# Kernel optimization log

Hardware: AMD Instinct MI355X
Metric: run time of the kernel (lower is better)

## Reference

```python
import jax, jax.numpy as jnp
import numpy as np

N_NODES = 100000
N_EDGES = 1600000
IN_FEATS = 128
N_HIDDEN = 128
N_CLASSES = 16


def setup_inputs() -> dict:
    key = jax.random.key(0)
    ks = jax.random.split(key, 10)
    features = jax.random.normal(ks[0], (N_NODES, IN_FEATS), dtype=jnp.float32)
    src = jax.random.randint(ks[1], (N_EDGES,), 0, N_NODES, dtype=jnp.int32)
    dst = jax.random.randint(ks[2], (N_EDGES,), 0, N_NODES, dtype=jnp.int32)
    # Glorot-ish init for the three GraphConv layers
    def glorot(k, fan_in, fan_out):
        s = (2.0 / (fan_in + fan_out)) ** 0.5
        return jax.random.normal(k, (fan_in, fan_out), dtype=jnp.float32) * s
    W0 = glorot(ks[3], IN_FEATS, N_HIDDEN)
    b0 = jnp.zeros((N_HIDDEN,), jnp.float32)
    W1 = glorot(ks[4], N_HIDDEN, N_HIDDEN)
    b1 = jnp.zeros((N_HIDDEN,), jnp.float32)
    W2 = glorot(ks[5], N_HIDDEN, N_CLASSES)
    b2 = jnp.zeros((N_CLASSES,), jnp.float32)
    return {"features": features, "src": src, "dst": dst,
            "W0": W0, "b0": b0, "W1": W1, "b1": b1, "W2": W2, "b2": b2}


def _graph_conv(h, src, dst, src_norm, dst_norm, W, b, act):
    # DGL GraphConv, norm='both':
    # out = D_dst^{-1/2} * sum_{(u->v) in E} (D_src^{-1/2} h)_u W  + b
    h = h * src_norm[:, None]           # [N, F] scale by out-degree^-1/2
    hw = h @ W                          # [N, F_out] transform before gather (F_out <= F here)
    agg = jax.ops.segment_sum(hw[src], dst, num_segments=h.shape[0])  # scatter-add over edges
    out = agg * dst_norm[:, None] + b
    return act(out)


def reference(features, src, dst, W0, b0, W1, b1, W2, b2):
    N = features.shape[0]
    ones = jnp.ones(src.shape[0], dtype=jnp.float32)
    out_deg = jnp.clip(jax.ops.segment_sum(ones, src, num_segments=N), 1.0)
    in_deg = jnp.clip(jax.ops.segment_sum(ones, dst, num_segments=N), 1.0)
    src_norm = out_deg ** -0.5
    dst_norm = in_deg ** -0.5

    relu = jax.nn.relu
    pos_sigmoid = lambda x: jax.nn.sigmoid(x) + 1e-8

    h = features.astype(jnp.float32)
    h = _graph_conv(h, src, dst, src_norm, dst_norm, W0, b0, relu)
    h = _graph_conv(h, src, dst, src_norm, dst_norm, W1, b1, relu)
    h = _graph_conv(h, src, dst, src_norm, dst_norm, W2, b2, pos_sigmoid)
    return h
```

## Files before the change

### kernel.cpp

```cpp
#include <hip/hip_runtime.h>
#include <hip/hip_bf16.h>


constexpr int BLK = 256;
constexpr int CH = 8192;

typedef __attribute__((ext_vector_type(8))) short s8v;
typedef __attribute__((ext_vector_type(4))) float f4v;

__device__ __forceinline__ float bflo(unsigned int u) { return __uint_as_float(u << 16); }
__device__ __forceinline__ float bfhi(unsigned int u) { return __uint_as_float(u & 0xffff0000u); }
__device__ __forceinline__ unsigned int bfr(float f) {
    unsigned int u = __float_as_uint(f);
    return (u + 0x7fffu + ((u >> 16) & 1u)) >> 16;
}
__device__ __forceinline__ unsigned int bfpack(float lo, float hi) {
    unsigned int ul = __float_as_uint(lo), uh = __float_as_uint(hi);
    unsigned int rl = (ul + 0x7fffu + ((ul >> 16) & 1u)) >> 16;
    unsigned int rh = (uh + 0x7fffu + ((uh >> 16) & 1u)) & 0xffff0000u;
    return rl | rh;
}

__global__ __launch_bounds__(256) void k_pcount(const int* __restrict__ src, const int* __restrict__ dst,
                                                int* __restrict__ pmat_d, int* __restrict__ pmat_s,
                                                int E, int NB) {
    __shared__ int hd[1024], hs[1024];
    for (int i = threadIdx.x; i < 1024; i += 256) { hd[i] = 0; hs[i] = 0; }
    __syncthreads();
    int b = blockIdx.x;
    int e0 = b * CH, e1 = min(e0 + CH, E);
    for (int e = e0 + threadIdx.x; e < e1; e += 256) {
        atomicAdd(&hd[dst[e] >> 7], 1);
        atomicAdd(&hs[src[e] >> 7], 1);
    }
    __syncthreads();
    for (int i = threadIdx.x; i < NB; i += 256) {
        pmat_d[(size_t)b * NB + i] = hd[i];
        pmat_s[(size_t)b * NB + i] = hs[i];
    }
}

__global__ __launch_bounds__(1024) void k_pscan1(const int* __restrict__ pmat_d, const int* __restrict__ pmat_s,
                                                 int* __restrict__ bbase_d, int* __restrict__ bbase_s,
                                                 int NB, int nblk) {
    const int* pmat = blockIdx.x ? pmat_s : pmat_d;
    int* bbase = blockIdx.x ? bbase_s : bbase_d;
    __shared__ int s[1024];
    int t = threadIdx.x;
    int tot = 0;
    if (t < NB) {
#pragma unroll 8
        for (int b = 0; b < nblk; b++) tot += pmat[(size_t)b * NB + t];
    }
    s[t] = (t < NB) ? tot : 0;
    __syncthreads();
    for (int d = 1; d < 1024; d <<= 1) {
        int x = (t >= d) ? s[t - d] : 0;
        __syncthreads();
        s[t] += x;
        __syncthreads();
    }
    if (t < NB) {
        bbase[t] = s[t] - tot;
        if (t == NB - 1) bbase[NB] = s[t];
    }
}

__global__ __launch_bounds__(256) void k_pscan2(const int* __restrict__ pmat_d, const int* __restrict__ pmat_s,
                                                const int* __restrict__ bbase_d, const int* __restrict__ bbase_s,
                                                int* __restrict__ omat_d, int* __restrict__ omat_s,
                                                int NB, int nblk) {
    int which = blockIdx.x & 1;
    int t = (blockIdx.x >> 1) * 256 + threadIdx.x;
    const int* pmat = which ? pmat_s : pmat_d;
    const int* bbase = which ? bbase_s : bbase_d;
    int* omat = which ? omat_s : omat_d;
    if (t >= NB) return;
    int run = bbase[t];
#pragma unroll 8
    for (int b = 0; b < nblk; b++) {
        size_t idx = (size_t)b * NB + t;
        omat[idx] = run;
        run += pmat[idx];
    }
}

__global__ __launch_bounds__(256) void k_pscatter(const int* __restrict__ src, const int* __restrict__ dst,
                                                  const int* __restrict__ omat_d, const int* __restrict__ omat_s,
                                                  unsigned int* __restrict__ ebuf_d, unsigned char* __restrict__ ebuf_s,
                                                  int E, int NB) {
    __shared__ int cd[1024], cs[1024];
    int b = blockIdx.x;
    for (int i = threadIdx.x; i < NB; i += 256) {
        cd[i] = omat_d[(size_t)b * NB + i];
        cs[i] = omat_s[(size_t)b * NB + i];
    }
    __syncthreads();
    int e0 = b * CH, e1 = min(e0 + CH, E);
    for (int e = e0 + threadIdx.x; e < e1; e += 256) {
        int s_ = src[e], d_ = dst[e];
        int pd = atomicAdd(&cd[d_ >> 7], 1);
        ebuf_d[pd] = (unsigned)s_ | ((unsigned)(d_ & 127) << 17);
        int ps = atomicAdd(&cs[s_ >> 7], 1);
        ebuf_s[ps] = (unsigned char)(s_ & 127);
    }
}

__global__ __launch_bounds__(256) void k_bcount(const unsigned char* __restrict__ ebuf_s,
                                                const int* __restrict__ bbase_s,
                                                float* __restrict__ srcn, int N) {
    __shared__ int cnt[128];
    int k = blockIdx.x;
    if (threadIdx.x < 128) cnt[threadIdx.x] = 0;
    __syncthreads();
    int beg = bbase_s[k], end = bbase_s[k + 1];
    for (int i = beg + threadIdx.x; i < end; i += 256) atomicAdd(&cnt[ebuf_s[i]], 1);
    __syncthreads();
    if (threadIdx.x < 128) {
        int v = k * 128 + threadIdx.x;
        if (v < N) {
            int c = cnt[threadIdx.x];
            if (c < 1) c = 1;
            srcn[v] = rsqrtf((float)c);
        }
    }
}

__global__ __launch_bounds__(256) void k_sortcsr(const unsigned int* __restrict__ ebuf,
                                                 const int* __restrict__ bbase,
                                                 int* __restrict__ csr, int* __restrict__ rowptr,
                                                 int N, int E) {
    __shared__ unsigned int rec[4096];
    __shared__ unsigned int sorted[4096];
    __shared__ int cnt[128];
    __shared__ int wstart[129];
    __shared__ int wcur[128];
    int k = blockIdx.x, tx = threadIdx.x;
    int ebeg = bbase[k];
    int ecnt = bbase[k + 1] - ebeg;
    if (ecnt > 4096) ecnt = 4096;
    if (tx < 128) cnt[tx] = 0;
    __syncthreads();
    for (int i = tx; i < ecnt; i += 256) {
        unsigned int r = ebuf[ebeg + i];
        rec[i] = r;
        atomicAdd(&cnt[(r >> 17) & 127], 1);
    }
    __syncthreads();
    if (tx < 128) wcur[tx] = cnt[tx];
    __syncthreads();
    for (int d = 1; d < 128; d <<= 1) {
        int x = (tx < 128 && tx >= d) ? wcur[tx - d] : 0;
        __syncthreads();
        if (tx < 128) wcur[tx] += x;
        __syncthreads();
    }
    if (tx < 128) wstart[tx] = wcur[tx] - cnt[tx];
    if (tx == 127) wstart[128] = wcur[127];
    __syncthreads();
    if (tx < 128) wcur[tx] = wstart[tx];
    __syncthreads();
    for (int i = tx; i < ecnt; i += 256) {
        unsigned int r = rec[i];
        int p = atomicAdd(&wcur[(r >> 17) & 127], 1);
        sorted[p] = r & 0x1FFFFu;
    }
    __syncthreads();
    for (int i = tx; i < ecnt; i += 256) csr[ebeg + i] = (int)sorted[i];
    if (tx < 128) {
        int v = k * 128 + tx;
        if (v < N) rowptr[v] = ebeg + wstart[tx];
    }
    if (k == (int)gridDim.x - 1 && tx == 0) rowptr[N] = E;
}

__global__ void k_wt3(const float* __restrict__ W0, const float* __restrict__ W1, const float* __restrict__ W2,
                      unsigned short* __restrict__ Wt0, unsigned short* __restrict__ Wt1,
                      unsigned short* __restrict__ Wt2) {
    int b = blockIdx.x;
    const float* W; unsigned short* Wt; int total, base;
    if (b < 64)      { W = W0; Wt = Wt0; total = 16384; base = b * 256; }
    else if (b < 128){ W = W1; Wt = Wt1; total = 16384; base = (b - 64) * 256; }
    else             { W = W2; Wt = Wt2; total = 2048;  base = (b - 128) * 256; }
    int i = base + threadIdx.x;
    if (i < total) {
        int Ncol = total >> 7;
        int c = i >> 7, k = i & 127;
        Wt[i] = (unsigned short)bfr(W[k * Ncol + c]);
    }
}

template <int NT, int F32IN>
__global__ __launch_bounds__(256) void k_gemm_mfma(const unsigned short* __restrict__ Ab,
                                                   const float* __restrict__ Af,
                                                   const float* __restrict__ srcn,
                                                   const unsigned short* __restrict__ Wt,
                                                   unsigned short* __restrict__ outb, int M) {
    __shared__ unsigned short As[64 * 128];
    __shared__ unsigned short Ws[NT * 16 * 128];
    int tx = threadIdx.x;
    int row0 = blockIdx.x * 64;
    for (int p = 0; p < NT; ++p) {
        int r = p * 16 + (tx >> 4);
        int c = tx & 15;
        int cs = c ^ (r & 7);
        *(uint4*)(&Ws[(r * 16 + cs) * 8]) = *(const uint4*)(Wt + (size_t)r * 128 + c * 8);
    }
    for (int p = 0; p < 4; ++p) {
        int r = p * 16 + (tx >> 4);
        int c = tx & 15;
        int cs = c ^ (r & 7);
        int gr = row0 + r;
        uint4 v = make_uint4(0u, 0u, 0u, 0u);
        if (gr < M) {
            if (F32IN) {
                const float4* pf = (const float4*)(Af + (size_t)gr * 128 + c * 8);
                float4 a = pf[0], b = pf[1];
                float s = srcn[gr];
                v.x = bfpack(a.x * s, a.y * s);
                v.y = bfpack(a.z * s, a.w * s);
                v.z = bfpack(b.x * s, b.y * s);
                v.w = bfpack(b.z * s, b.w * s);
            } else {
                v = *(const uint4*)(Ab + (size_t)gr * 128 + c * 8);
            }
        }
        *(uint4*)(&As[(r * 16 + cs) * 8]) = v;
    }
    __syncthreads();

    int w = tx >> 6, l = tx & 63;
    int lr = l & 15, lg = l >> 4;
    f4v acc[NT];
#pragma unroll
    for (int nt = 0; nt < NT; ++nt) { acc[nt][0] = 0.f; acc[nt][1] = 0.f; acc[nt][2] = 0.f; acc[nt][3] = 0.f; }

    int ar = w * 16 + lr;
#pragma unroll
    for (int kk = 0; kk < 4; ++kk) {
        s8v af = *(const s8v*)(&As[(ar * 16 + ((kk * 4 + lg) ^ (ar & 7))) * 8]);
#pragma unroll
        for (int nt = 0; nt < NT; ++nt) {
            int br = nt * 16 + lr;
            s8v bf = *(const s8v*)(&Ws[(br * 16 + ((kk * 4 + lg) ^ (br & 7))) * 8]);
            acc[nt] = __builtin_amdgcn_mfma_f32_16x16x32_bf16(af, bf, acc[nt], 0, 0, 0);
        }
    }
#pragma unroll
    for (int nt = 0; nt < NT; ++nt) {
#pragma unroll
        for (int i = 0; i < 4; ++i) {
            int R = row0 + w * 16 + lg * 4 + i;
            if (R < M) {
                int col = nt * 16 + lr;
                outb[(size_t)R * (NT * 16) + col] = (unsigned short)bfr(acc[nt][i]);
            }
        }
    }
}

__global__ __launch_bounds__(256) void k_aggN(const unsigned short* __restrict__ hw,
                                              const int* __restrict__ csr,
                                              const int* __restrict__ rowptr,
                                              const float* __restrict__ srcn,
                                              const float* __restrict__ bias,
                                              unsigned short* __restrict__ out, int N) {
    int t = blockIdx.x * 256 + threadIdx.x;
    int v = t >> 4, sub = t & 15;
    if (v >= N) return;
    int s0 = rowptr[v], s1 = rowptr[v + 1];

    float a0 = 0.f, a1 = 0.f, a2 = 0.f, a3 = 0.f, a4 = 0.f, a5 = 0.f, a6 = 0.f, a7 = 0.f;
#define ACC8(V)                                                         \
    a0 += bflo(V.x); a1 += bfhi(V.x); a2 += bflo(V.y); a3 += bfhi(V.y); \
    a4 += bflo(V.z); a5 += bfhi(V.z); a6 += bflo(V.w); a7 += bfhi(V.w);
    int e = s0;
    for (; e + 4 <= s1; e += 4) {
        int x0 = csr[e], x1 = csr[e + 1], x2 = csr[e + 2], x3 = csr[e + 3];
        uint4 v0 = *(const uint4*)(hw + (size_t)x0 * 128 + sub * 8);
        uint4 v1 = *(const uint4*)(hw + (size_t)x1 * 128 + sub * 8);
        uint4 v2 = *(const uint4*)(hw + (size_t)x2 * 128 + sub * 8);
        uint4 v3 = *(const uint4*)(hw + (size_t)x3 * 128 + sub * 8);
        ACC8(v0) ACC8(v1) ACC8(v2) ACC8(v3)
    }
    for (; e < s1; ++e) {
        int x0 = csr[e];
        uint4 v0 = *(const uint4*)(hw + (size_t)x0 * 128 + sub * 8);
        ACC8(v0)
    }
#undef ACC8
    int deg = s1 - s0;
    if (deg < 1) deg = 1;
    float dn = rsqrtf((float)deg);
    float4 b0 = *(const float4*)(bias + sub * 8);
    float4 b1 = *(const float4*)(bias + sub * 8 + 4);
    float sn = srcn[v];
    float o0 = fmaxf(a0 * dn + b0.x, 0.f) * sn, o1 = fmaxf(a1 * dn + b0.y, 0.f) * sn;
    float o2 = fmaxf(a2 * dn + b0.z, 0.f) * sn, o3 = fmaxf(a3 * dn + b0.w, 0.f) * sn;
    float o4 = fmaxf(a4 * dn + b1.x, 0.f) * sn, o5 = fmaxf(a5 * dn + b1.y, 0.f) * sn;
    float o6 = fmaxf(a6 * dn + b1.z, 0.f) * sn, o7 = fmaxf(a7 * dn + b1.w, 0.f) * sn;
    uint4 o;
    o.x = bfpack(o0, o1); o.y = bfpack(o2, o3);
    o.z = bfpack(o4, o5); o.w = bfpack(o6, o7);
    *(uint4*)(out + (size_t)v * 128 + sub * 8) = o;
}

__global__ __launch_bounds__(256) void k_agg16(const unsigned short* __restrict__ hw,
                                               const int* __restrict__ csr,
                                               const int* __restrict__ rowptr,
                                               const float* __restrict__ bias,
                                               float* __restrict__ out, int N) {
    int t = blockIdx.x * 256 + threadIdx.x;
    int v = t >> 2, q = t & 3;
    if (v >= N) return;
    int s0 = rowptr[v], s1 = rowptr[v + 1];
    float a0 = 0.f, a1 = 0.f, a2 = 0.f, a3 = 0.f;
#define ACC4(V)                                                         \
    a0 += bflo(V.x); a1 += bfhi(V.x); a2 += bflo(V.y); a3 += bfhi(V.y);
    int e = s0;
    for (; e + 4 <= s1; e += 4) {
        int x0 = csr[e], x1 = csr[e + 1], x2 = csr[e + 2], x3 = csr[e + 3];
        uint2 v0 = *(const uint2*)(hw + (size_t)x0 * 16 + q * 4);
        uint2 v1 = *(const uint2*)(hw + (size_t)x1 * 16 + q * 4);
        uint2 v2 = *(const uint2*)(hw + (size_t)x2 * 16 + q * 4);
        uint2 v3 = *(const uint2*)(hw + (size_t)x3 * 16 + q * 4);
        ACC4(v0) ACC4(v1) ACC4(v2) ACC4(v3)
    }
    for (; e < s1; ++e) {
        int x0 = csr[e];
        uint2 v0 = *(const uint2*)(hw + (size_t)x0 * 16 + q * 4);
        ACC4(v0)
    }
#undef ACC4
    int deg = s1 - s0;
    if (deg < 1) deg = 1;
    float dn = rsqrtf((float)deg);
    float4 b = *(const float4*)(bias + q * 4);
    float o0 = 1.f / (1.f + __expf(-(a0 * dn + b.x))) + 1e-8f;
    float o1 = 1.f / (1.f + __expf(-(a1 * dn + b.y))) + 1e-8f;
    float o2 = 1.f / (1.f + __expf(-(a2 * dn + b.z))) + 1e-8f;
    float o3 = 1.f / (1.f + __expf(-(a3 * dn + b.w))) + 1e-8f;
    *(float4*)(out + (size_t)v * 16 + q * 4) = make_float4(o0, o1, o2, o3);
}

extern "C" void kernel_launch(void* const* d_in, const int* in_sizes, int n_in,
                              void* d_out, int out_size, void* d_ws, size_t ws_size,
                              hipStream_t stream) {
    const float* features = (const float*)d_in[0];
    const int*   src      = (const int*)d_in[1];
    const int*   dst      = (const int*)d_in[2];
    const float* W0       = (const float*)d_in[3];
    const float* b0       = (const float*)d_in[4];
    const float* W1       = (const float*)d_in[5];
    const float* b1       = (const float*)d_in[6];
    const float* W2       = (const float*)d_in[7];
    const float* b2       = (const float*)d_in[8];
    float* out = (float*)d_out;

    const int N = in_sizes[0] / 128;
    const int E = in_sizes[1];
    const int NB = (N + 127) >> 7;
    const int nblk = (E + CH - 1) / CH;

    char* ws = (char*)d_ws;
    size_t off = 0;
    auto alloc = [&](size_t bytes) -> char* {
        char* p = ws + off;
        off += (bytes + 255) / 256 * 256;
        return p;
    };
    int* pmat_d  = (int*)alloc((size_t)nblk * NB * 4);
    int* pmat_s  = (int*)alloc((size_t)nblk * NB * 4);
    int* omat_d  = (int*)alloc((size_t)nblk * NB * 4);
    int* omat_s  = (int*)alloc((size_t)nblk * NB * 4);
    int* bbase_d = (int*)alloc((size_t)(NB + 1) * 4);
    int* bbase_s = (int*)alloc((size_t)(NB + 1) * 4);
    unsigned int*  ebuf_d = (unsigned int*)alloc((size_t)E * 4);
    unsigned char* ebuf_s = (unsigned char*)alloc((size_t)E);
    int* csr     = (int*)alloc((size_t)E * 4);
    int* rowptr  = (int*)alloc((size_t)(N + 1) * 4);
    float* srcn  = (float*)alloc((size_t)N * 4);
    unsigned short* Wt0 = (unsigned short*)alloc(128 * 128 * 2);
    unsigned short* Wt1 = (unsigned short*)alloc(128 * 128 * 2);
    unsigned short* Wt2 = (unsigned short*)alloc(16 * 128 * 2);
    unsigned short* B1 = (unsigned short*)alloc((size_t)N * 128 * 2);
    unsigned short* B2 = (unsigned short*)alloc((size_t)N * 128 * 2);
    unsigned short* HW16 = (unsigned short*)alloc((size_t)N * 16 * 2);
    (void)ws_size; (void)n_in; (void)out_size;

    k_pcount<<<nblk, 256, 0, stream>>>(src, dst, pmat_d, pmat_s, E, NB);
    k_pscan1<<<2, 1024, 0, stream>>>(pmat_d, pmat_s, bbase_d, bbase_s, NB, nblk);
    k_pscan2<<<2 * ((NB + 255) / 256), 256, 0, stream>>>(pmat_d, pmat_s, bbase_d, bbase_s, omat_d, omat_s, NB, nblk);
    k_pscatter<<<nblk, 256, 0, stream>>>(src, dst, omat_d, omat_s, ebuf_d, ebuf_s, E, NB);
    k_bcount<<<NB, 256, 0, stream>>>(ebuf_s, bbase_s, srcn, N);
    k_sortcsr<<<NB, 256, 0, stream>>>(ebuf_d, bbase_d, csr, rowptr, N, E);
    k_wt3<<<136, 256, 0, stream>>>(W0, W1, W2, Wt0, Wt1, Wt2);

    int gb = (N + 63) / 64;
    int anb = (N * 16 + 255) / 256;
    int a16b = (N * 4 + 255) / 256;

    k_gemm_mfma<8, 1><<<gb, 256, 0, stream>>>(nullptr, features, srcn, Wt0, B2, N);
    k_aggN<<<anb, 256, 0, stream>>>(B2, csr, rowptr, srcn, b0, B1, N);
    k_gemm_mfma<8, 0><<<gb, 256, 0, stream>>>(B1, nullptr, nullptr, Wt1, B2, N);
    k_aggN<<<anb, 256, 0, stream>>>(B2, csr, rowptr, srcn, b1, B1, N);
    k_gemm_mfma<1, 0><<<gb, 256, 0, stream>>>(B1, nullptr, nullptr, Wt2, HW16, N);
    k_agg16<<<a16b, 256, 0, stream>>>(HW16, csr, rowptr, b2, out, N);
}
```

Before: 351.7 us.

## Sort nodes by in-degree for aggregation and load GEMM A operands directly

Adds a counting sort of nodes by in-degree (histogram, scan, scatter) that produces a permutation, so that the aggregation kernels process nodes with similar degree together and wavefront divergence shrinks. The GEMM now reads A fragments straight from global memory into registers instead of staging them in LDS, and each wave computes two 16-row tiles, so a block covers 128 rows. The aggN gather loop is unrolled from 4 to 8 loads to keep more memory requests in flight. This costs three extra small launches, and the permuted order makes node accesses in aggregation less contiguous.

```diff
diff --git a/kernel.cpp b/kernel.cpp
--- a/kernel.cpp
+++ b/kernel.cpp
@@ -4,6 +4,7 @@
 
 constexpr int BLK = 256;
 constexpr int CH = 8192;
+constexpr int DCH = 8192;
 
 typedef __attribute__((ext_vector_type(8))) short s8v;
 typedef __attribute__((ext_vector_type(4))) float f4v;
@@ -174,6 +175,52 @@
     if (k == (int)gridDim.x - 1 && tx == 0) rowptr[N] = E;
 }
 
+__global__ __launch_bounds__(256) void k_dhist(const int* __restrict__ rowptr, int* __restrict__ dpart, int N) {
+    __shared__ int h[128];
+    if (threadIdx.x < 128) h[threadIdx.x] = 0;
+    __syncthreads();
+    int n0 = blockIdx.x * DCH, n1 = min(n0 + DCH, N);
+    for (int n = n0 + threadIdx.x; n < n1; n += 256) {
+        int deg = rowptr[n + 1] - rowptr[n];
+        atomicAdd(&h[min(deg, 127)], 1);
+    }
+    __syncthreads();
+    if (threadIdx.x < 128) dpart[blockIdx.x * 128 + threadIdx.x] = h[threadIdx.x];
+}
+
+__global__ __launch_bounds__(128) void k_dscan(const int* __restrict__ dpart, int* __restrict__ dmat, int nchunk) {
+    __shared__ int s[128];
+    int t = threadIdx.x;
+    int tot = 0;
+    for (int b = 0; b < nchunk; b++) tot += dpart[b * 128 + t];
+    s[t] = tot;
+    __syncthreads();
+    for (int d = 1; d < 128; d <<= 1) {
+        int x = (t >= d) ? s[t - d] : 0;
+        __syncthreads();
+        s[t] += x;
+        __syncthreads();
+    }
+    int run = s[t] - tot;
+    for (int b = 0; b < nchunk; b++) {
+        dmat[b * 128 + t] = run;
+        run += dpart[b * 128 + t];
+    }
+}
+
+__global__ __launch_bounds__(256) void k_dscatter(const int* __restrict__ rowptr, const int* __restrict__ dmat,
+                                                  int* __restrict__ perm, int N) {
+    __shared__ int cur[128];
+    if (threadIdx.x < 128) cur[threadIdx.x] = dmat[blockIdx.x * 128 + threadIdx.x];
+    __syncthreads();
+    int n0 = blockIdx.x * DCH, n1 = min(n0 + DCH, N);
+    for (int n = n0 + threadIdx.x; n < n1; n += 256) {
+        int deg = rowptr[n + 1] - rowptr[n];
+        int p = atomicAdd(&cur[min(deg, 127)], 1);
+        perm[p] = n;
+    }
+}
+
 __global__ void k_wt3(const float* __restrict__ W0, const float* __restrict__ W1, const float* __restrict__ W2,
                       unsigned short* __restrict__ Wt0, unsigned short* __restrict__ Wt1,
                       unsigned short* __restrict__ Wt2) {
@@ -196,64 +243,73 @@
                                                    const float* __restrict__ srcn,
                                                    const unsigned short* __restrict__ Wt,
                                                    unsigned short* __restrict__ outb, int M) {
-    __shared__ unsigned short As[64 * 128];
     __shared__ unsigned short Ws[NT * 16 * 128];
     int tx = threadIdx.x;
-    int row0 = blockIdx.x * 64;
     for (int p = 0; p < NT; ++p) {
         int r = p * 16 + (tx >> 4);
         int c = tx & 15;
         int cs = c ^ (r & 7);
         *(uint4*)(&Ws[(r * 16 + cs) * 8]) = *(const uint4*)(Wt + (size_t)r * 128 + c * 8);
     }
-    for (int p = 0; p < 4; ++p) {
-        int r = p * 16 + (tx >> 4);
-        int c = tx & 15;
-        int cs = c ^ (r & 7);
-        int gr = row0 + r;
-        uint4 v = make_uint4(0u, 0u, 0u, 0u);
-        if (gr < M) {
-            if (F32IN) {
-                const float4* pf = (const float4*)(Af + (size_t)gr * 128 + c * 8);
-                float4 a = pf[0], b = pf[1];
-                float s = srcn[gr];
-                v.x = bfpack(a.x * s, a.y * s);
-                v.y = bfpack(a.z * s, a.w * s);
-                v.z = bfpack(b.x * s, b.y * s);
-                v.w = bfpack(b.z * s, b.w * s);
-            } else {
-                v = *(const uint4*)(Ab + (size_t)gr * 128 + c * 8);
-            }
-        }
-        *(uint4*)(&As[(r * 16 + cs) * 8]) = v;
-    }
     __syncthreads();
 
     int w = tx >> 6, l = tx & 63;
     int lr = l & 15, lg = l >> 4;
-    f4v acc[NT];
-#pragma unroll
-    for (int nt = 0; nt < NT; ++nt) { acc[nt][0] = 0.f; acc[nt][1] = 0.f; acc[nt][2] = 0.f; acc[nt][3] = 0.f; }
-
-    int ar = w * 16 + lr;
+    int row_base = blockIdx.x * 128;
+    int r0 = row_base + (w * 2 + 0) * 16 + lr;
+    int r1 = row_base + (w * 2 + 1) * 16 + lr;
+    bool m0 = r0 < M, m1 = r1 < M;
+    float sn0 = 1.f, sn1 = 1.f;
+    if (F32IN) { sn0 = m0 ? srcn[r0] : 0.f; sn1 = m1 ? srcn[r1] : 0.f; }
+
+    f4v acc[2][NT];
+#pragma unroll
+    for (int s = 0; s < 2; ++s)
+#pragma unroll
+        for (int nt = 0; nt < NT; ++nt) { acc[s][nt][0] = 0.f; acc[s][nt][1] = 0.f; acc[s][nt][2] = 0.f; acc[s][nt][3] = 0.f; }
+
 #pragma unroll
     for (int kk = 0; kk < 4; ++kk) {
-        s8v af = *(const s8v*)(&As[(ar * 16 + ((kk * 4 + lg) ^ (ar & 7))) * 8]);
+        int off = (kk * 4 + lg) * 8;
+        union { uint4 u; s8v v; } a0, a1;
+        a0.u = make_uint4(0u, 0u, 0u, 0u);
+        a1.u = make_uint4(0u, 0u, 0u, 0u);
+        if (F32IN) {
+            if (m0) {
+                const float4* pf = (const float4*)(Af + (size_t)r0 * 128 + off);
+                float4 x = pf[0], y = pf[1];
+                a0.u.x = bfpack(x.x * sn0, x.y * sn0); a0.u.y = bfpack(x.z * sn0, x.w * sn0);
+                a0.u.z = bfpack(y.x * sn0, y.y * sn0); a0.u.w = bfpack(y.z * sn0, y.w * sn0);
+            }
+            if (m1) {
+                const float4* pf = (const float4*)(Af + (size_t)r1 * 128 + off);
+                float4 x = pf[0], y = pf[1];
+                a1.u.x = bfpack(x.x * sn1, x.y * sn1); a1.u.y = bfpack(x.z * sn1, x.w * sn1);
+                a1.u.z = bfpack(y.x * sn1, y.y * sn1); a1.u.w = bfpack(y.z * sn1, y.w * sn1);
+            }
+        } else {
+            if (m0) a0.u = *(const uint4*)(Ab + (size_t)r0 * 128 + off);
+            if (m1) a1.u = *(const uint4*)(Ab + (size_t)r1 * 128 + off);
+        }
 #pragma unroll
         for (int nt = 0; nt < NT; ++nt) {
             int br = nt * 16 + lr;
             s8v bf = *(const s8v*)(&Ws[(br * 16 + ((kk * 4 + lg) ^ (br & 7))) * 8]);
-            acc[nt] = __builtin_amdgcn_mfma_f32_16x16x32_bf16(af, bf, acc[nt], 0, 0, 0);
+            acc[0][nt] = __builtin_amdgcn_mfma_f32_16x16x32_bf16(a0.v, bf, acc[0][nt], 0, 0, 0);
+            acc[1][nt] = __builtin_amdgcn_mfma_f32_16x16x32_bf16(a1.v, bf, acc[1][nt], 0, 0, 0);
         }
     }
 #pragma unroll
-    for (int nt = 0; nt < NT; ++nt) {
-#pragma unroll
-        for (int i = 0; i < 4; ++i) {
-            int R = row0 + w * 16 + lg * 4 + i;
-            if (R < M) {
-                int col = nt * 16 + lr;
-                outb[(size_t)R * (NT * 16) + col] = (unsigned short)bfr(acc[nt][i]);
+    for (int s = 0; s < 2; ++s) {
+#pragma unroll
+        for (int nt = 0; nt < NT; ++nt) {
+#pragma unroll
+            for (int i = 0; i < 4; ++i) {
+                int R = row_base + (w * 2 + s) * 16 + lg * 4 + i;
+                if (R < M) {
+                    int col = nt * 16 + lr;
+                    outb[(size_t)R * (NT * 16) + col] = (unsigned short)bfr(acc[s][nt][i]);
+                }
             }
         }
     }
@@ -262,30 +318,38 @@
 __global__ __launch_bounds__(256) void k_aggN(const unsigned short* __restrict__ hw,
                                               const int* __restrict__ csr,
                                               const int* __restrict__ rowptr,
+                                              const int* __restrict__ perm,
                                               const float* __restrict__ srcn,
                                               const float* __restrict__ bias,
                                               unsigned short* __restrict__ out, int N) {
     int t = blockIdx.x * 256 + threadIdx.x;
-    int v = t >> 4, sub = t & 15;
-    if (v >= N) return;
+    int vi = t >> 4, sub = t & 15;
+    if (vi >= N) return;
+    int v = perm[vi];
     int s0 = rowptr[v], s1 = rowptr[v + 1];
+    const unsigned short* hws = hw + sub * 8;
 
     float a0 = 0.f, a1 = 0.f, a2 = 0.f, a3 = 0.f, a4 = 0.f, a5 = 0.f, a6 = 0.f, a7 = 0.f;
 #define ACC8(V)                                                         \
     a0 += bflo(V.x); a1 += bfhi(V.x); a2 += bflo(V.y); a3 += bfhi(V.y); \
     a4 += bflo(V.z); a5 += bfhi(V.z); a6 += bflo(V.w); a7 += bfhi(V.w);
     int e = s0;
-    for (; e + 4 <= s1; e += 4) {
-        int x0 = csr[e], x1 = csr[e + 1], x2 = csr[e + 2], x3 = csr[e + 3];
-        uint4 v0 = *(const uint4*)(hw + (size_t)x0 * 128 + sub * 8);
-        uint4 v1 = *(const uint4*)(hw + (size_t)x1 * 128 + sub * 8);
-        uint4 v2 = *(const uint4*)(hw + (size_t)x2 * 128 + sub * 8);
-        uint4 v3 = *(const uint4*)(hw + (size_t)x3 * 128 + sub * 8);
-        ACC8(v0) ACC8(v1) ACC8(v2) ACC8(v3)
+    for (; e + 8 <= s1; e += 8) {
+        int x0 = csr[e],     x1 = csr[e + 1], x2 = csr[e + 2], x3 = csr[e + 3];
+        int x4 = csr[e + 4], x5 = csr[e + 5], x6 = csr[e + 6], x7 = csr[e + 7];
+        uint4 v0 = *(const uint4*)(hws + (size_t)x0 * 128);
+        uint4 v1 = *(const uint4*)(hws + (size_t)x1 * 128);
+        uint4 v2 = *(const uint4*)(hws + (size_t)x2 * 128);
+        uint4 v3 = *(const uint4*)(hws + (size_t)x3 * 128);
+        uint4 v4 = *(const uint4*)(hws + (size_t)x4 * 128);
+        uint4 v5 = *(const uint4*)(hws + (size_t)x5 * 128);
+        uint4 v6 = *(const uint4*)(hws + (size_t)x6 * 128);
+        uint4 v7 = *(const uint4*)(hws + (size_t)x7 * 128);
+        ACC8(v0) ACC8(v1) ACC8(v2) ACC8(v3) ACC8(v4) ACC8(v5) ACC8(v6) ACC8(v7)
     }
     for (; e < s1; ++e) {
         int x0 = csr[e];
-        uint4 v0 = *(const uint4*)(hw + (size_t)x0 * 128 + sub * 8);
+        uint4 v0 = *(const uint4*)(hws + (size_t)x0 * 128);
         ACC8(v0)
     }
 #undef ACC8
@@ -308,27 +372,30 @@
 __global__ __launch_bounds__(256) void k_agg16(const unsigned short* __restrict__ hw,
                                                const int* __restrict__ csr,
                                                const int* __restrict__ rowptr,
+                                               const int* __restrict__ perm,
                                                const float* __restrict__ bias,
                                                float* __restrict__ out, int N) {
     int t = blockIdx.x * 256 + threadIdx.x;
-    int v = t >> 2, q = t & 3;
-    if (v >= N) return;
+    int vi = t >> 2, q = t & 3;
+    if (vi >= N) return;
+    int v = perm[vi];
     int s0 = rowptr[v], s1 = rowptr[v + 1];
+    const unsigned short* hws = hw + q * 4;
     float a0 = 0.f, a1 = 0.f, a2 = 0.f, a3 = 0.f;
 #define ACC4(V)                                                         \
     a0 += bflo(V.x); a1 += bfhi(V.x); a2 += bflo(V.y); a3 += bfhi(V.y);
     int e = s0;
     for (; e + 4 <= s1; e += 4) {
         int x0 = csr[e], x1 = csr[e + 1], x2 = csr[e + 2], x3 = csr[e + 3];
-        uint2 v0 = *(const uint2*)(hw + (size_t)x0 * 16 + q * 4);
-        uint2 v1 = *(const uint2*)(hw + (size_t)x1 * 16 + q * 4);
-        uint2 v2 = *(const uint2*)(hw + (size_t)x2 * 16 + q * 4);
-        uint2 v3 = *(const uint2*)(hw + (size_t)x3 * 16 + q * 4);
+        uint2 v0 = *(const uint2*)(hws + (size_t)x0 * 16);
+        uint2 v1 = *(const uint2*)(hws + (size_t)x1 * 16);
+        uint2 v2 = *(const uint2*)(hws + (size_t)x2 * 16);
+        uint2 v3 = *(const uint2*)(hws + (size_t)x3 * 16);
         ACC4(v0) ACC4(v1) ACC4(v2) ACC4(v3)
     }
     for (; e < s1; ++e) {
         int x0 = csr[e];
-        uint2 v0 = *(const uint2*)(hw + (size_t)x0 * 16 + q * 4);
+        uint2 v0 = *(const uint2*)(hws + (size_t)x0 * 16);
         ACC4(v0)
     }
 #undef ACC4
@@ -361,6 +428,7 @@
     const int E = in_sizes[1];
     const int NB = (N + 127) >> 7;
     const int nblk = (E + CH - 1) / CH;
+    const int dnb = (N + DCH - 1) / DCH;
 
     char* ws = (char*)d_ws;
     size_t off = 0;
@@ -380,6 +448,9 @@
     int* csr     = (int*)alloc((size_t)E * 4);
     int* rowptr  = (int*)alloc((size_t)(N + 1) * 4);
     float* srcn  = (float*)alloc((size_t)N * 4);
+    int* dpart   = (int*)alloc((size_t)dnb * 128 * 4);
+    int* dmat    = (int*)alloc((size_t)dnb * 128 * 4);
+    int* perm    = (int*)alloc((size_t)N * 4);
     unsigned short* Wt0 = (unsigned short*)alloc(128 * 128 * 2);
     unsigned short* Wt1 = (unsigned short*)alloc(128 * 128 * 2);
     unsigned short* Wt2 = (unsigned short*)alloc(16 * 128 * 2);
@@ -394,16 +465,19 @@
     k_pscatter<<<nblk, 256, 0, stream>>>(src, dst, omat_d, omat_s, ebuf_d, ebuf_s, E, NB);
     k_bcount<<<NB, 256, 0, stream>>>(ebuf_s, bbase_s, srcn, N);
     k_sortcsr<<<NB, 256, 0, stream>>>(ebuf_d, bbase_d, csr, rowptr, N, E);
+    k_dhist<<<dnb, 256, 0, stream>>>(rowptr, dpart, N);
+    k_dscan<<<1, 128, 0, stream>>>(dpart, dmat, dnb);
+    k_dscatter<<<dnb, 256, 0, stream>>>(rowptr, dmat, perm, N);
     k_wt3<<<136, 256, 0, stream>>>(W0, W1, W2, Wt0, Wt1, Wt2);
 
-    int gb = (N + 63) / 64;
+    int gb = (N + 127) / 128;
     int anb = (N * 16 + 255) / 256;
     int a16b = (N * 4 + 255) / 256;
 
     k_gemm_mfma<8, 1><<<gb, 256, 0, stream>>>(nullptr, features, srcn, Wt0, B2, N);
-    k_aggN<<<anb, 256, 0, stream>>>(B2, csr, rowptr, srcn, b0, B1, N);
+    k_aggN<<<anb, 256, 0, stream>>>(B2, csr, rowptr, perm, srcn, b0, B1, N);
     k_gemm_mfma<8, 0><<<gb, 256, 0, stream>>>(B1, nullptr, nullptr, Wt1, B2, N);
-    k_aggN<<<anb, 256, 0, stream>>>(B2, csr, rowptr, srcn, b1, B1, N);
+    k_aggN<<<anb, 256, 0, stream>>>(B2, csr, rowptr, perm, srcn, b1, B1, N);
     k_gemm_mfma<1, 0><<<gb, 256, 0, stream>>>(B1, nullptr, nullptr, Wt2, HW16, N);
-    k_agg16<<<a16b, 256, 0, stream>>>(HW16, csr, rowptr, b2, out, N);
-}
+    k_agg16<<<a16b, 256, 0, stream>>>(HW16, csr, rowptr, perm, b2, out, N);
+}
```

Result: slower. 385.3 us (+9.6%).
